# Optimization experiments

Hardware: AMD Instinct MI355X
Metric: run time of the kernel (lower is better)

The kernel has to match this reference:

```python
import jax, jax.numpy as jnp
import numpy as np

REG_CONST = 0.05  # matches init_kwargs reg_const


def setup_inputs() -> dict:
    key = jax.random.key(0)
    k1, k2, k3 = jax.random.split(key, 3)
    N, D, C = 1_000_000, 128, 10
    X_train = jax.random.normal(k1, (N, D), dtype=jnp.float32)
    y_train = jax.random.randint(k2, (N,), 0, C)
    w = jax.random.normal(k3, (C, D), dtype=jnp.float32) * 0.01
    return {"X_train": X_train, "y_train": y_train, "w": w}


def reference(X_train, y_train, w):
    """Vectorized SVM.calc_gradient: multiclass hinge loss + gradient w.r.t. w.

    Original loops over samples i and classes c:
      margin = scores[c] - scores[y_i] + 1; if margin > 0 (c != y_i):
        loss += margin; grad[y_i] += X[i]; grad[c] -= X[i]
    then loss /= N (+ 0.5*reg*||w||^2), grad /= N (+ reg*w).
    (The original seeds `gradients` with np.random.rand -- a bug; we use the
    intended zero init so the math is deterministic.)
    """
    N = X_train.shape[0]
    C = w.shape[0]
    inv_n = jnp.asarray(1.0 / N, dtype=X_train.dtype)

    scores = X_train @ w.T                                        # [N, C]
    correct = jnp.take_along_axis(scores, y_train[:, None], axis=1)  # [N, 1]
    margins = scores - correct + 1.0                              # [N, C]
    onehot = jax.nn.one_hot(y_train, C, dtype=scores.dtype)       # [N, C]
    mask = jnp.where((margins > 0) & (onehot == 0), 1.0, 0.0).astype(scores.dtype)

    loss = jnp.sum(mask * margins) * inv_n + 0.5 * REG_CONST * jnp.sum(w * w)

    # grad[c] gets -X[i] for each violating (i, c); grad[y_i] gets +X[i] per
    # violating class -> counts[i] copies of X[i] scatter-added to row y_i.
    counts = mask.sum(axis=1)                                     # [N]
    neg_part = mask.T @ X_train                                   # [C, D]
    pos_part = jax.ops.segment_sum(counts[:, None] * X_train, y_train,
                                   num_segments=C)                # [C, D]
    gradients = (pos_part - neg_part) * inv_n + REG_CONST * w
    return gradients, loss
```

## Files before the change

kernel.cpp:

```cpp
#include <hip/hip_runtime.h>

#define REG_CONST 0.05f
#define NCLASS 10
#define DIM 128
#define TILE 32
#define NBLOCKS 1024
#define NTHREADS 256

template <int CTRL>
__device__ __forceinline__ float dpp_mov(float x) {
  return __int_as_float(
      __builtin_amdgcn_update_dpp(0, __float_as_int(x), CTRL, 0xF, 0xF, true));
}

__global__ __launch_bounds__(NTHREADS, 2)
void svm_fused(const float* __restrict__ X, const int* __restrict__ y,
               const float* __restrict__ w, float* __restrict__ out,
               int ntiles, float inv_n) {
  __shared__ float4 coefs[2][TILE * 3];
  __shared__ float4 red[5 * 256];
  __shared__ float  lred[4];

  const int t  = threadIdx.x;
  const int l  = t & 63;
  const int wv = t >> 6;

  const int o  = t & 15;
  const int rq = t >> 4;
  const int d4 = t & 31;
  const int rg = t >> 5;

  const float4* X4 = (const float4*)X;
  const float4* W4 = (const float4*)w;

  float4 g[NCLASS];
  #pragma unroll
  for (int c = 0; c < NCLASS; ++c) g[c] = make_float4(0.f, 0.f, 0.f, 0.f);
  float loss_acc = 0.f;

  int prev_row0 = 0;
  int have = 0;
  int p = 0;

  for (int tix = blockIdx.x; tix < ntiles; tix += gridDim.x) {
    const int row0 = tix * TILE;

    #pragma unroll
    for (int pass = 0; pass < 2; ++pass) {
      const int rr  = (pass << 4) + rq;
      const int row = row0 + rr;
      const float4 xa = X4[(size_t)row * 32 + o];
      const float4 xc = X4[(size_t)row * 32 + o + 16];
      const int yv = y[row];

      float s[NCLASS];
      #pragma unroll
      for (int c = 0; c < NCLASS; ++c) {
        const float4 wa = W4[c * 32 + o];
        const float4 wc = W4[c * 32 + o + 16];
        float v = fmaf(xa.x, wa.x, fmaf(xa.y, wa.y,
                  fmaf(xa.z, wa.z, xa.w * wa.w)));
        v = fmaf(xc.x, wc.x, fmaf(xc.y, wc.y,
            fmaf(xc.z, wc.z, fmaf(xc.w, wc.w, v))));
        s[c] = v;
      }
      #pragma unroll
      for (int c = 0; c < NCLASS; ++c) {
        s[c] += dpp_mov<0xB1>(s[c]);
        s[c] += dpp_mov<0x4E>(s[c]);
        s[c] += __shfl_xor(s[c], 4);
        s[c] += dpp_mov<0x128>(s[c]);
      }

      float sy = s[0];
      #pragma unroll
      for (int c = 1; c < NCLASS; ++c) sy = (c == yv) ? s[c] : sy;

      float cnt = 0.f, rl = 0.f;
      float cf[NCLASS];
      #pragma unroll
      for (int c = 0; c < NCLASS; ++c) {
        float mg = s[c] - sy + 1.0f;
        bool act = (mg > 0.f) && (c != yv);
        cf[c] = act ? -1.f : 0.f;
        cnt += act ? 1.f : 0.f;
        rl  += act ? mg : 0.f;
      }
      #pragma unroll
      for (int c = 0; c < NCLASS; ++c) cf[c] = (c == yv) ? cnt : cf[c];

      if (o == 0) {
        coefs[p][rr * 3 + 0] = make_float4(cf[0], cf[1], cf[2], cf[3]);
        coefs[p][rr * 3 + 1] = make_float4(cf[4], cf[5], cf[6], cf[7]);
        coefs[p][rr * 3 + 2] = make_float4(cf[8], cf[9], 0.f, 0.f);
        loss_acc += rl;
      }
    }

    if (have) {
      const float4* cb = coefs[p ^ 1];
      #pragma unroll
      for (int k = 0; k < 4; ++k) {
        const int r = (k << 3) + rg;
        const float4 x4 = X4[(size_t)(prev_row0 + r) * 32 + d4];
        const float4 c0 = cb[r * 3 + 0];
        const float4 c1 = cb[r * 3 + 1];
        const float4 c2 = cb[r * 3 + 2];
#define ACC4(cc, gi)                         \
        g[gi].x = fmaf(cc, x4.x, g[gi].x);   \
        g[gi].y = fmaf(cc, x4.y, g[gi].y);   \
        g[gi].z = fmaf(cc, x4.z, g[gi].z);   \
        g[gi].w = fmaf(cc, x4.w, g[gi].w);
        ACC4(c0.x, 0) ACC4(c0.y, 1) ACC4(c0.z, 2) ACC4(c0.w, 3)
        ACC4(c1.x, 4) ACC4(c1.y, 5) ACC4(c1.z, 6) ACC4(c1.w, 7)
        ACC4(c2.x, 8) ACC4(c2.y, 9)
#undef ACC4
      }
    }

    __syncthreads();
    prev_row0 = row0;
    have = 1;
    p ^= 1;
  }

  if (have) {
    const float4* cb = coefs[p ^ 1];
    #pragma unroll
    for (int k = 0; k < 4; ++k) {
      const int r = (k << 3) + rg;
      const float4 x4 = X4[(size_t)(prev_row0 + r) * 32 + d4];
      const float4 c0 = cb[r * 3 + 0];
      const float4 c1 = cb[r * 3 + 1];
      const float4 c2 = cb[r * 3 + 2];
#define ACC4(cc, gi)                         \
      g[gi].x = fmaf(cc, x4.x, g[gi].x);     \
      g[gi].y = fmaf(cc, x4.y, g[gi].y);     \
      g[gi].z = fmaf(cc, x4.z, g[gi].z);     \
      g[gi].w = fmaf(cc, x4.w, g[gi].w);
      ACC4(c0.x, 0) ACC4(c0.y, 1) ACC4(c0.z, 2) ACC4(c0.w, 3)
      ACC4(c1.x, 4) ACC4(c1.y, 5) ACC4(c1.z, 6) ACC4(c1.w, 7)
      ACC4(c2.x, 8) ACC4(c2.y, 9)
#undef ACC4
    }
  }

  float contrib = loss_acc * inv_n;
  if (blockIdx.x == 0) {
    float rw = 0.f;
    for (int i = t; i < NCLASS * DIM; i += NTHREADS) rw = fmaf(w[i], w[i], rw);
    contrib = fmaf(0.5f * REG_CONST, rw, contrib);
  }
  #pragma unroll
  for (int off = 32; off; off >>= 1) contrib += __shfl_down(contrib, off);
  if (l == 0) lred[wv] = contrib;
  __syncthreads();
  if (t == 0) atomicAdd(out + NCLASS * DIM, lred[0] + lred[1] + lred[2] + lred[3]);

  #pragma unroll
  for (int chunk = 0; chunk < 2; ++chunk) {
    __syncthreads();
    #pragma unroll
    for (int k = 0; k < 5; ++k) red[k * 256 + t] = g[chunk * 5 + k];
    __syncthreads();
    if (t < 160) {
      int k = t >> 5, dd = t & 31;
      float sx = 0.f, syy = 0.f, sz = 0.f, sw = 0.f;
      #pragma unroll
      for (int r8 = 0; r8 < 8; ++r8) {
        float4 v = red[k * 256 + (r8 << 5) + dd];
        sx += v.x; syy += v.y; sz += v.z; sw += v.w;
      }
      int c = chunk * 5 + k;
      int base = c * DIM + (dd << 2);
      float ax = sx * inv_n, ay = syy * inv_n, az = sz * inv_n, aw = sw * inv_n;
      if (blockIdx.x == 0) {
        ax += REG_CONST * w[base + 0];
        ay += REG_CONST * w[base + 1];
        az += REG_CONST * w[base + 2];
        aw += REG_CONST * w[base + 3];
      }
      atomicAdd(out + base + 0, ax);
      atomicAdd(out + base + 1, ay);
      atomicAdd(out + base + 2, az);
      atomicAdd(out + base + 3, aw);
    }
  }
}

extern "C" void kernel_launch(void* const* d_in, const int* in_sizes, int n_in,
                              void* d_out, int out_size, void* d_ws, size_t ws_size,
                              hipStream_t stream) {
  const float* X = (const float*)d_in[0];
  const int*   y = (const int*)d_in[1];
  const float* w = (const float*)d_in[2];
  float* out = (float*)d_out;
  int N = in_sizes[1];
  int ntiles = N / TILE;
  float inv_n = 1.0f / (float)N;
  hipMemsetAsync(d_out, 0, (size_t)out_size * sizeof(float), stream);
  svm_fused<<<NBLOCKS, NTHREADS, 0, stream>>>(X, y, w, out, ntiles, inv_n);
}
```

Before: 794.8 us.

## Accumulate gradients directly from register-resident rows, dropping second X read and LDS coefs

Each thread now keeps the row slice it loaded for scoring and uses it directly for the gradient accumulation. This removes the second global read of X, the shared-memory coefficient double buffer and the per-tile __syncthreads. The next row is prefetched into registers while the current one is processed, and the shfl_xor(4) step becomes a DPP row shift. In exchange each thread holds 80 float accumulators instead of 40, which raises register pressure, and the final reduction now goes through cross-lane shuffles plus an LDS pass. The grid is halved to 512 blocks.

Result: faster. 761.3 us (-4.2%).

```diff
diff --git a/kernel.cpp b/kernel.cpp
--- a/kernel.cpp
+++ b/kernel.cpp
@@ -3,8 +3,8 @@
 #define REG_CONST 0.05f
 #define NCLASS 10
 #define DIM 128
-#define TILE 32
-#define NBLOCKS 1024
+#define RSTEP 16
+#define NBLOCKS 512
 #define NTHREADS 256
 
 template <int CTRL>
@@ -16,134 +16,113 @@
 __global__ __launch_bounds__(NTHREADS, 2)
 void svm_fused(const float* __restrict__ X, const int* __restrict__ y,
                const float* __restrict__ w, float* __restrict__ out,
-               int ntiles, float inv_n) {
-  __shared__ float4 coefs[2][TILE * 3];
-  __shared__ float4 red[5 * 256];
+               int nsteps, float inv_n) {
+  __shared__ float4 red[1280];
   __shared__ float  lred[4];
 
   const int t  = threadIdx.x;
   const int l  = t & 63;
   const int wv = t >> 6;
-
   const int o  = t & 15;
   const int rq = t >> 4;
-  const int d4 = t & 31;
-  const int rg = t >> 5;
 
   const float4* X4 = (const float4*)X;
   const float4* W4 = (const float4*)w;
 
-  float4 g[NCLASS];
+  float4 g[NCLASS][2];
   #pragma unroll
-  for (int c = 0; c < NCLASS; ++c) g[c] = make_float4(0.f, 0.f, 0.f, 0.f);
+  for (int c = 0; c < NCLASS; ++c) {
+    g[c][0] = make_float4(0.f, 0.f, 0.f, 0.f);
+    g[c][1] = make_float4(0.f, 0.f, 0.f, 0.f);
+  }
   float loss_acc = 0.f;
 
-  int prev_row0 = 0;
-  int have = 0;
-  int p = 0;
+  int row = blockIdx.x * RSTEP + rq;
+  float4 xa = X4[(size_t)row * 32 + o];
+  float4 xc = X4[(size_t)row * 32 + o + 16];
+  int yv = y[row];
+  const int stride_rows = gridDim.x * RSTEP;
 
-  for (int tix = blockIdx.x; tix < ntiles; tix += gridDim.x) {
-    const int row0 = tix * TILE;
+  for (int s = blockIdx.x; s < nsteps; s += gridDim.x) {
+    const int rown = row + stride_rows;
+    const int pr   = ((s + gridDim.x) < nsteps) ? rown : rq;
+    const float4 xan = X4[(size_t)pr * 32 + o];
+    const float4 xcn = X4[(size_t)pr * 32 + o + 16];
+    const int    yvn = y[pr];
+
+    float sc[NCLASS];
+    #pragma unroll
+    for (int c = 0; c < NCLASS; ++c) {
+      const float4 wa = W4[c * 32 + o];
+      const float4 wc = W4[c * 32 + o + 16];
+      float v = fmaf(xa.x, wa.x, fmaf(xa.y, wa.y,
+                fmaf(xa.z, wa.z, xa.w * wa.w)));
+      v = fmaf(xc.x, wc.x, fmaf(xc.y, wc.y,
+          fmaf(xc.z, wc.z, fmaf(xc.w, wc.w, v))));
+      sc[c] = v;
+    }
+    #pragma unroll
+    for (int c = 0; c < NCLASS; ++c) {
+      sc[c] += dpp_mov<0xB1>(sc[c]);
+      sc[c] += dpp_mov<0x4E>(sc[c]);
+      sc[c] += dpp_mov<0x124>(sc[c]);
+      sc[c] += dpp_mov<0x128>(sc[c]);
+    }
+
+    const float sy0 = sc[0];
+    float sy = sy0;
+    #pragma unroll
+    for (int c = 1; c < NCLASS; ++c) sy = (c == yv) ? sc[c] : sy;
+
+    float cnt = 0.f, rl = 0.f;
+    float cf[NCLASS];
+    #pragma unroll
+    for (int c = 0; c < NCLASS; ++c) {
+      const float mg = sc[c] - sy + 1.0f;
+      const bool act = (mg > 0.f) && (c != yv);
+      cf[c] = act ? -1.f : 0.f;
+      cnt += act ? 1.f : 0.f;
+      rl  += act ? mg : 0.f;
+    }
+    #pragma unroll
+    for (int c = 0; c < NCLASS; ++c) cf[c] = (c == yv) ? cnt : cf[c];
+    if (o == 0) loss_acc += rl;
 
     #pragma unroll
-    for (int pass = 0; pass < 2; ++pass) {
-      const int rr  = (pass << 4) + rq;
-      const int row = row0 + rr;
-      const float4 xa = X4[(size_t)row * 32 + o];
-      const float4 xc = X4[(size_t)row * 32 + o + 16];
-      const int yv = y[row];
-
-      float s[NCLASS];
-      #pragma unroll
-      for (int c = 0; c < NCLASS; ++c) {
-        const float4 wa = W4[c * 32 + o];
-        const float4 wc = W4[c * 32 + o + 16];
-        float v = fmaf(xa.x, wa.x, fmaf(xa.y, wa.y,
-                  fmaf(xa.z, wa.z, xa.w * wa.w)));
-        v = fmaf(xc.x, wc.x, fmaf(xc.y, wc.y,
-            fmaf(xc.z, wc.z, fmaf(xc.w, wc.w, v))));
-        s[c] = v;
-      }
-      #pragma unroll
-      for (int c = 0; c < NCLASS; ++c) {
-        s[c] += dpp_mov<0xB1>(s[c]);
-        s[c] += dpp_mov<0x4E>(s[c]);
-        s[c] += __shfl_xor(s[c], 4);
-        s[c] += dpp_mov<0x128>(s[c]);
-      }
-
-      float sy = s[0];
-      #pragma unroll
-      for (int c = 1; c < NCLASS; ++c) sy = (c == yv) ? s[c] : sy;
-
-      float cnt = 0.f, rl = 0.f;
-      float cf[NCLASS];
-      #pragma unroll
-      for (int c = 0; c < NCLASS; ++c) {
-        float mg = s[c] - sy + 1.0f;
-        bool act = (mg > 0.f) && (c != yv);
-        cf[c] = act ? -1.f : 0.f;
-        cnt += act ? 1.f : 0.f;
-        rl  += act ? mg : 0.f;
-      }
-      #pragma unroll
-      for (int c = 0; c < NCLASS; ++c) cf[c] = (c == yv) ? cnt : cf[c];
-
-      if (o == 0) {
-        coefs[p][rr * 3 + 0] = make_float4(cf[0], cf[1], cf[2], cf[3]);
-        coefs[p][rr * 3 + 1] = make_float4(cf[4], cf[5], cf[6], cf[7]);
-        coefs[p][rr * 3 + 2] = make_float4(cf[8], cf[9], 0.f, 0.f);
-        loss_acc += rl;
-      }
+    for (int c = 0; c < NCLASS; ++c) {
+      g[c][0].x = fmaf(cf[c], xa.x, g[c][0].x);
+      g[c][0].y = fmaf(cf[c], xa.y, g[c][0].y);
+      g[c][0].z = fmaf(cf[c], xa.z, g[c][0].z);
+      g[c][0].w = fmaf(cf[c], xa.w, g[c][0].w);
+      g[c][1].x = fmaf(cf[c], xc.x, g[c][1].x);
+      g[c][1].y = fmaf(cf[c], xc.y, g[c][1].y);
+      g[c][1].z = fmaf(cf[c], xc.z, g[c][1].z);
+      g[c][1].w = fmaf(cf[c], xc.w, g[c][1].w);
     }
 
-    if (have) {
-      const float4* cb = coefs[p ^ 1];
-      #pragma unroll
-      for (int k = 0; k < 4; ++k) {
-        const int r = (k << 3) + rg;
-        const float4 x4 = X4[(size_t)(prev_row0 + r) * 32 + d4];
-        const float4 c0 = cb[r * 3 + 0];
-        const float4 c1 = cb[r * 3 + 1];
-        const float4 c2 = cb[r * 3 + 2];
-#define ACC4(cc, gi)                         \
-        g[gi].x = fmaf(cc, x4.x, g[gi].x);   \
-        g[gi].y = fmaf(cc, x4.y, g[gi].y);   \
-        g[gi].z = fmaf(cc, x4.z, g[gi].z);   \
-        g[gi].w = fmaf(cc, x4.w, g[gi].w);
-        ACC4(c0.x, 0) ACC4(c0.y, 1) ACC4(c0.z, 2) ACC4(c0.w, 3)
-        ACC4(c1.x, 4) ACC4(c1.y, 5) ACC4(c1.z, 6) ACC4(c1.w, 7)
-        ACC4(c2.x, 8) ACC4(c2.y, 9)
-#undef ACC4
-      }
-    }
-
-    __syncthreads();
-    prev_row0 = row0;
-    have = 1;
-    p ^= 1;
+    xa = xan; xc = xcn; yv = yvn; row = rown;
   }
 
-  if (have) {
-    const float4* cb = coefs[p ^ 1];
+  #pragma unroll
+  for (int c = 0; c < NCLASS; ++c) {
     #pragma unroll
-    for (int k = 0; k < 4; ++k) {
-      const int r = (k << 3) + rg;
-      const float4 x4 = X4[(size_t)(prev_row0 + r) * 32 + d4];
-      const float4 c0 = cb[r * 3 + 0];
-      const float4 c1 = cb[r * 3 + 1];
-      const float4 c2 = cb[r * 3 + 2];
-#define ACC4(cc, gi)                         \
-      g[gi].x = fmaf(cc, x4.x, g[gi].x);     \
-      g[gi].y = fmaf(cc, x4.y, g[gi].y);     \
-      g[gi].z = fmaf(cc, x4.z, g[gi].z);     \
-      g[gi].w = fmaf(cc, x4.w, g[gi].w);
-      ACC4(c0.x, 0) ACC4(c0.y, 1) ACC4(c0.z, 2) ACC4(c0.w, 3)
-      ACC4(c1.x, 4) ACC4(c1.y, 5) ACC4(c1.z, 6) ACC4(c1.w, 7)
-      ACC4(c2.x, 8) ACC4(c2.y, 9)
-#undef ACC4
+    for (int h = 0; h < 2; ++h) {
+      float4 v = g[c][h];
+      v.x += __shfl_xor(v.x, 16); v.y += __shfl_xor(v.y, 16);
+      v.z += __shfl_xor(v.z, 16); v.w += __shfl_xor(v.w, 16);
+      v.x += __shfl_xor(v.x, 32); v.y += __shfl_xor(v.y, 32);
+      v.z += __shfl_xor(v.z, 32); v.w += __shfl_xor(v.w, 32);
+      g[c][h] = v;
     }
   }
+  if (l < 16) {
+    #pragma unroll
+    for (int c = 0; c < NCLASS; ++c) {
+      red[wv * 320 + l * 20 + c * 2 + 0] = g[c][0];
+      red[wv * 320 + l * 20 + c * 2 + 1] = g[c][1];
+    }
+  }
+  __syncthreads();
 
   float contrib = loss_acc * inv_n;
   if (blockIdx.x == 0) {
@@ -157,34 +136,31 @@
   __syncthreads();
   if (t == 0) atomicAdd(out + NCLASS * DIM, lred[0] + lred[1] + lred[2] + lred[3]);
 
-  #pragma unroll
-  for (int chunk = 0; chunk < 2; ++chunk) {
-    __syncthreads();
-    #pragma unroll
-    for (int k = 0; k < 5; ++k) red[k * 256 + t] = g[chunk * 5 + k];
-    __syncthreads();
-    if (t < 160) {
-      int k = t >> 5, dd = t & 31;
-      float sx = 0.f, syy = 0.f, sz = 0.f, sw = 0.f;
-      #pragma unroll
-      for (int r8 = 0; r8 < 8; ++r8) {
-        float4 v = red[k * 256 + (r8 << 5) + dd];
-        sx += v.x; syy += v.y; sz += v.z; sw += v.w;
-      }
-      int c = chunk * 5 + k;
-      int base = c * DIM + (dd << 2);
-      float ax = sx * inv_n, ay = syy * inv_n, az = sz * inv_n, aw = sw * inv_n;
-      if (blockIdx.x == 0) {
-        ax += REG_CONST * w[base + 0];
-        ay += REG_CONST * w[base + 1];
-        az += REG_CONST * w[base + 2];
-        aw += REG_CONST * w[base + 3];
-      }
-      atomicAdd(out + base + 0, ax);
-      atomicAdd(out + base + 1, ay);
-      atomicAdd(out + base + 2, az);
-      atomicAdd(out + base + 3, aw);
+  for (int idx = t; idx < 320; idx += NTHREADS) {
+    const float4 a = red[idx];
+    const float4 b = red[320 + idx];
+    const float4 cc = red[640 + idx];
+    const float4 d = red[960 + idx];
+    float sx = a.x + b.x + cc.x + d.x;
+    float sy2 = a.y + b.y + cc.y + d.y;
+    float sz = a.z + b.z + cc.z + d.z;
+    float sw = a.w + b.w + cc.w + d.w;
+    const int oo = idx / 20;
+    const int k  = idx % 20;
+    const int c  = k >> 1;
+    const int h  = k & 1;
+    const int base = c * DIM + (oo + 16 * h) * 4;
+    float ax = sx * inv_n, ay = sy2 * inv_n, az = sz * inv_n, aw = sw * inv_n;
+    if (blockIdx.x == 0) {
+      ax += REG_CONST * w[base + 0];
+      ay += REG_CONST * w[base + 1];
+      az += REG_CONST * w[base + 2];
+      aw += REG_CONST * w[base + 3];
     }
+    atomicAdd(out + base + 0, ax);
+    atomicAdd(out + base + 1, ay);
+    atomicAdd(out + base + 2, az);
+    atomicAdd(out + base + 3, aw);
   }
 }
 
@@ -196,8 +172,8 @@
   const float* w = (const float*)d_in[2];
   float* out = (float*)d_out;
   int N = in_sizes[1];
-  int ntiles = N / TILE;
+  int nsteps = N / RSTEP;
   float inv_n = 1.0f / (float)N;
   hipMemsetAsync(d_out, 0, (size_t)out_size * sizeof(float), stream);
-  svm_fused<<<NBLOCKS, NTHREADS, 0, stream>>>(X, y, w, out, ntiles, inv_n);
+  svm_fused<<<NBLOCKS, NTHREADS, 0, stream>>>(X, y, w, out, nsteps, inv_n);
 }
```
